# Performance work log

Hardware: AMD Instinct MI355X
Metric: run time of the kernel (lower is better)

The kernel has to match this reference:

```python
import jax, jax.numpy as jnp
import numpy as np

EPS = 1e-5  # torch nn.LayerNorm default eps
DIST_CUTOFF = 10.0


def _ln(x, g, b):
    m = jnp.mean(x, axis=-1, keepdims=True)
    v = jnp.mean((x - m) ** 2, axis=-1, keepdims=True)
    return (x - m) * jax.lax.rsqrt(v + EPS) * g + b


def setup_inputs() -> dict:
    key = jax.random.key(0)
    ks = iter(jax.random.split(key, 48))
    L, B, N, D, H = 4, 1, 256, 128, 512
    IN = D + N  # 384 == node_dim + edge_dim + node_dim under the consistency constraint
    r = lambda *s: jax.random.normal(next(ks), s, jnp.float32) * 0.02
    return dict(
        nodes=jax.random.normal(next(ks), (B, N, D), jnp.float32),
        coords=jax.random.normal(next(ks), (B, N, 3), jnp.float32),
        ee_w=r(1, D), ee_b=jnp.zeros(D), ee_g=jnp.ones(D), ee_bt=jnp.zeros(D),
        nu1_w=r(L, IN, H), nu1_b=jnp.zeros((L, H)), nu_g=jnp.ones((L, H)), nu_bt=jnp.zeros((L, H)),
        nu2_w=r(L, H, D), nu2_b=jnp.zeros((L, D)),
        eu1_w=r(L, IN, H), eu1_b=jnp.zeros((L, H)), eu_g=jnp.ones((L, H)), eu_bt=jnp.zeros((L, H)),
        eu2_w=r(L, H, D), eu2_b=jnp.zeros((L, D)),
        sp1_w=r(D, H), sp1_b=jnp.zeros(H), sp_g=jnp.ones(H), sp_bt=jnp.zeros(H),
        sp2_w=r(H, 3), sp2_b=jnp.zeros(3),
        no1_w=r(D, H), no1_b=jnp.zeros(H), no_g=jnp.ones(H), no_bt=jnp.zeros(H),
        no2_w=r(H, D), no2_b=jnp.zeros(D),
    )


def reference(nodes, coords, ee_w, ee_b, ee_g, ee_bt,
              nu1_w, nu1_b, nu_g, nu_bt, nu2_w, nu2_b,
              eu1_w, eu1_b, eu_g, eu_bt, eu2_w, eu2_b,
              sp1_w, sp1_b, sp_g, sp_bt, sp2_w, sp2_b,
              no1_w, no1_b, no_g, no_bt, no2_w, no2_b):
    B, N, D = nodes.shape
    # initialize_edges: pairwise distances -> edge embedding + adjacency
    diff = coords[:, :, None, :] - coords[:, None, :, :]           # [B,N,N,3]
    sq = jnp.sum(diff * diff, axis=-1)                              # [B,N,N]
    dist = jnp.where(sq > 0, jnp.sqrt(jnp.where(sq > 0, sq, 1.0)), 0.0)
    adj = (dist < DIST_CUTOFF).astype(nodes.dtype)                  # [B,N,N]
    edges = jax.nn.relu(_ln(dist[..., None] @ ee_w + ee_b, ee_g, ee_bt))  # [B,N,N,D]

    def step(carry, p):
        nd, ed = carry
        w1n, b1n, gn, btn, w2n, b2n, w1e, b1e, ge, bte, w2e, b2e = p
        # messages: einsum('bijk,bik->bij', edges*adj[...,None], nodes)
        msgs = adj * jnp.einsum('bijk,bik->bij', ed, nd)            # [B,N,N]
        ni = jnp.concatenate([nd, msgs], axis=-1)                    # [B,N,D+N]
        nd_new = nd + jax.nn.relu(_ln(ni @ w1n + b1n, gn, btn)) @ w2n + b2n
        pairs = jnp.concatenate([
            jnp.broadcast_to(nd[:, :, None, :], (B, N, N, D)),
            jnp.broadcast_to(nd[:, None, :, :], (B, N, N, D))], axis=-1)  # [B,N,N,2D]
        ei = jnp.concatenate([ed, pairs], axis=-1)                   # [B,N,N,3D]
        ed_new = ed + jax.nn.relu(_ln(ei @ w1e + b1e, ge, bte)) @ w2e + b2e
        return (nd_new, ed_new), None

    (nd, _ed), _ = jax.lax.scan(
        step, (nodes, edges),
        (nu1_w, nu1_b, nu_g, nu_bt, nu2_w, nu2_b,
         eu1_w, eu1_b, eu_g, eu_bt, eu2_w, eu2_b))

    nodes_out = jax.nn.relu(_ln(nd @ no1_w + no1_b, no_g, no_bt)) @ no2_w + no2_b
    coords_pred = jax.nn.relu(_ln(nodes_out @ sp1_w + sp1_b, sp_g, sp_bt)) @ sp2_w + sp2_b
    return nodes_out, coords_pred
```

## Files before the change

kernel.cpp:

```cpp
#include <hip/hip_runtime.h>

#define LNEPS 1e-5f

typedef unsigned short ushort_t;
typedef __attribute__((ext_vector_type(8))) short short8;
typedef __attribute__((ext_vector_type(4))) float f32x4;

__device__ inline unsigned short f2b(float f) {
    union { float f; unsigned int u; } c; c.f = f;
    unsigned int u = c.u;
    unsigned int r = (u + 0x7FFFu + ((u >> 16) & 1u)) >> 16;
    return (unsigned short)r;
}

__global__ void k_convw(const float* __restrict__ w1, const float* __restrict__ w2,
                        ushort_t* __restrict__ w1P, ushort_t* __restrict__ w2P) {
    int idx = blockIdx.x * 256 + threadIdx.x;
    if (idx < 65536) {
        int l = idx >> 14, r = idx & 16383;
        int c = r >> 9;  r &= 511;
        int kb = r >> 6, lane = r & 63;
        int col = c * 16 + (lane & 15);
        int k0 = kb * 32 + (lane >> 4) * 8;
        ushort_t o[8];
        #pragma unroll
        for (int e = 0; e < 8; ++e) {
            int kl = k0 + e;
            int row = kl < 128 ? kl : kl + 128;
            o[e] = f2b(w1[((size_t)l * 384 + row) * 512 + col]);
        }
        *(uint4*)(w1P + (size_t)idx * 8) = *(uint4*)o;
    }
    if (idx < 32768) {
        int l = idx >> 13, r = idx & 8191;
        int c2 = r >> 10; r &= 1023;
        int kbg = r >> 6, lane = r & 63;
        int col = c2 * 16 + (lane & 15);
        int k0 = kbg * 32 + (lane >> 4) * 8;
        ushort_t o[8];
        #pragma unroll
        for (int e = 0; e < 8; ++e)
            o[e] = f2b(w2[((size_t)l * 512 + k0 + e) * 128 + col]);
        *(uint4*)(w2P + (size_t)idx * 8) = *(uint4*)o;
    }
}

__global__ void k_init(const float* __restrict__ coords,
                       const float* __restrict__ ee_w, const float* __restrict__ ee_b,
                       const float* __restrict__ ee_g, const float* __restrict__ ee_bt,
                       float* __restrict__ ed, float* __restrict__ adjf) {
    int r = blockIdx.x * 4 + (threadIdx.x >> 6);
    int lane = threadIdx.x & 63;
    int i = r >> 8, j = r & 255;
    float dx = coords[i * 3 + 0] - coords[j * 3 + 0];
    float dy = coords[i * 3 + 1] - coords[j * 3 + 1];
    float dz = coords[i * 3 + 2] - coords[j * 3 + 2];
    float sq = dx * dx + dy * dy + dz * dz;
    float dist = sq > 0.f ? sqrtf(sq) : 0.f;
    if (lane == 0) adjf[r] = dist < 10.f ? 1.f : 0.f;
    float e0 = dist * ee_w[lane] + ee_b[lane];
    float e1 = dist * ee_w[lane + 64] + ee_b[lane + 64];
    float s = e0 + e1, q = e0 * e0 + e1 * e1;
    #pragma unroll
    for (int off = 1; off < 64; off <<= 1) {
        s += __shfl_xor(s, off, 64);
        q += __shfl_xor(q, off, 64);
    }
    float mean = s * (1.f / 128.f);
    float var = q * (1.f / 128.f) - mean * mean;
    float rs = rsqrtf(var + LNEPS);
    ed[(size_t)r * 128 + lane]      = fmaxf((e0 - mean) * rs * ee_g[lane] + ee_bt[lane], 0.f);
    ed[(size_t)r * 128 + lane + 64] = fmaxf((e1 - mean) * rs * ee_g[lane + 64] + ee_bt[lane + 64], 0.f);
}

__global__ __launch_bounds__(512) void k_pre(
    const float* __restrict__ nd, const float* __restrict__ W1,
    const float* __restrict__ b1,
    float* __restrict__ cI, ushort_t* __restrict__ ndb) {
    __shared__ float ndl[128];
    int p = blockIdx.x, t = threadIdx.x;
    if (t < 128) {
        float v = nd[(size_t)p * 128 + t];
        ndl[t] = v;
        ndb[(size_t)p * 128 + t] = f2b(v);
    }
    __syncthreads();
    const float* wm = W1 + (size_t)128 * 512 + t;
    float a1 = b1[t];
    #pragma unroll 4
    for (int k = 0; k < 128; ++k) a1 += ndl[k] * wm[(size_t)k * 512];
    cI[(size_t)p * 512 + t] = a1;
}

__global__ void k_msgs(const float* __restrict__ ed, const float* __restrict__ nd,
                       const float* __restrict__ adjf, float* __restrict__ msgs) {
    int r = blockIdx.x * 4 + (threadIdx.x >> 6);
    int lane = threadIdx.x & 63;
    int i = r >> 8;
    const float* er = ed + (size_t)r * 128;
    const float* nr = nd + (size_t)i * 128;
    float sum = er[lane] * nr[lane] + er[lane + 64] * nr[lane + 64];
    #pragma unroll
    for (int off = 1; off < 64; off <<= 1) sum += __shfl_xor(sum, off, 64);
    if (lane == 0) msgs[r] = adjf[r] * sum;
}

__global__ __launch_bounds__(512) void k_mlp(
    const float* __restrict__ in0, int w0, const float* __restrict__ in1, int w1n,
    const float* __restrict__ W1, const float* __restrict__ b1,
    const float* __restrict__ g, const float* __restrict__ bt,
    const float* __restrict__ W2, const float* __restrict__ b2, int O,
    const float* __restrict__ res, float* __restrict__ out) {
    __shared__ float ni[384];
    __shared__ float hsh[512];
    __shared__ float part[4][128];
    __shared__ float red[16];
    int row = blockIdx.x;
    int t = threadIdx.x;
    int K = w0 + w1n;
    if (t < w0) ni[t] = in0[(size_t)row * w0 + t];
    else if (t < K) ni[t] = in1[(size_t)row * w1n + (t - w0)];
    __syncthreads();
    float acc = b1[t];
    #pragma unroll 4
    for (int k = 0; k < K; ++k) acc += ni[k] * W1[(size_t)k * 512 + t];
    float s = acc, q = acc * acc;
    #pragma unroll
    for (int off = 1; off < 64; off <<= 1) {
        s += __shfl_xor(s, off, 64);
        q += __shfl_xor(q, off, 64);
    }
    int wv = t >> 6;
    if ((t & 63) == 0) { red[wv] = s; red[8 + wv] = q; }
    __syncthreads();
    float S = 0.f, Q = 0.f;
    #pragma unroll
    for (int w = 0; w < 8; ++w) { S += red[w]; Q += red[8 + w]; }
    float mean = S * (1.f / 512.f);
    float var = Q * (1.f / 512.f) - mean * mean;
    float rs = rsqrtf(var + LNEPS);
    hsh[t] = fmaxf((acc - mean) * rs * g[t] + bt[t], 0.f);
    __syncthreads();
    int qd = t >> 7, c = t & 127;
    float pacc = 0.f;
    if (c < O) {
        #pragma unroll 4
        for (int kk = 0; kk < 128; ++kk)
            pacc += hsh[qd * 128 + kk] * W2[(size_t)(qd * 128 + kk) * O + c];
    }
    part[qd][c] = pacc;
    __syncthreads();
    if (t < O) {
        float v = part[0][t] + part[1][t] + part[2][t] + part[3][t] + b2[t];
        if (res) v += res[(size_t)row * O + t];
        out[(size_t)row * O + t] = v;
    }
}

__global__ __launch_bounds__(512, 4) void k_edge(
    float* ed, const ushort_t* __restrict__ ndb, const float* __restrict__ cIg,
    const ushort_t* __restrict__ w1P,
    const float* __restrict__ g, const float* __restrict__ bt,
    const ushort_t* __restrict__ w2P, const float* __restrict__ b2) {
    __shared__ char smem[70144];
    const int tid = threadIdx.x;
    const int w = tid >> 6, lane = tid & 63;
    const int l15 = lane & 15, lhi = lane >> 4;
    const int rbase = blockIdx.x * 64;
    const int ib = rbase >> 8;
    const int jbase = rbase & 255;

    #pragma unroll
    for (int it = 0; it < 4; ++it) {
        int c = tid + it * 512;
        int row = c >> 5, q = c & 31;
        uint4 pk;
        if (q < 16) {
            const float4* sp = (const float4*)(ed + (size_t)(rbase + row) * 128 + q * 8);
            float4 v0 = sp[0], v1 = sp[1];
            pk.x = (unsigned)f2b(v0.x) | ((unsigned)f2b(v0.y) << 16);
            pk.y = (unsigned)f2b(v0.z) | ((unsigned)f2b(v0.w) << 16);
            pk.z = (unsigned)f2b(v1.x) | ((unsigned)f2b(v1.y) << 16);
            pk.w = (unsigned)f2b(v1.z) | ((unsigned)f2b(v1.w) << 16);
        } else {
            pk = *(const uint4*)(ndb + (size_t)(jbase + row) * 128 + (q - 16) * 8);
        }
        *(uint4*)(smem + row * 512 + ((q ^ (row & 7)) * 16)) = pk;
    }
    __syncthreads();

    f32x4 acc[4][4];
    f32x4 zero = {0.f, 0.f, 0.f, 0.f};
    #pragma unroll
    for (int m = 0; m < 4; ++m)
        #pragma unroll
        for (int n = 0; n < 4; ++n) acc[m][n] = zero;

    const int cw = w * 64;
    #pragma unroll 2
    for (int kb = 0; kb < 8; ++kb) {
        short8 a[4];
        #pragma unroll
        for (int m = 0; m < 4; ++m) {
            int row = m * 16 + l15;
            a[m] = *(const short8*)(smem + row * 512 + (((kb * 4 + lhi) ^ (row & 7)) * 16));
        }
        #pragma unroll
        for (int n = 0; n < 4; ++n) {
            short8 b = *(const short8*)(w1P + ((((w * 4 + n) * 8 + kb) << 6) + lane) * 8);
            #pragma unroll
            for (int m = 0; m < 4; ++m)
                acc[m][n] = __builtin_amdgcn_mfma_f32_16x16x32_bf16(a[m], b, acc[m][n], 0, 0, 0);
        }
    }

    float* red = (float*)(smem + 65536);
    float* stats = (float*)(smem + 69632);
    {
        float ci[4];
        #pragma unroll
        for (int n = 0; n < 4; ++n) ci[n] = cIg[(size_t)ib * 512 + cw + n * 16 + l15];
        #pragma unroll
        for (int m = 0; m < 4; ++m) {
            float s[4] = {0.f, 0.f, 0.f, 0.f}, q[4] = {0.f, 0.f, 0.f, 0.f};
            #pragma unroll
            for (int n = 0; n < 4; ++n)
                #pragma unroll
                for (int e = 0; e < 4; ++e) {
                    float v = acc[m][n][e] + ci[n];
                    acc[m][n][e] = v;
                    s[e] += v; q[e] += v * v;
                }
            #pragma unroll
            for (int off = 1; off < 16; off <<= 1)
                #pragma unroll
                for (int e = 0; e < 4; ++e) {
                    s[e] += __shfl_xor(s[e], off, 64);
                    q[e] += __shfl_xor(q[e], off, 64);
                }
            if (l15 == 0) {
                #pragma unroll
                for (int e = 0; e < 4; ++e) {
                    int row = m * 16 + lhi * 4 + e;
                    red[(w * 64 + row) * 2 + 0] = s[e];
                    red[(w * 64 + row) * 2 + 1] = q[e];
                }
            }
        }
    }
    __syncthreads();
    if (tid < 64) {
        float S = 0.f, Q = 0.f;
        #pragma unroll
        for (int ww = 0; ww < 8; ++ww) {
            S += red[(ww * 64 + tid) * 2 + 0];
            Q += red[(ww * 64 + tid) * 2 + 1];
        }
        float mean = S * (1.f / 512.f);
        float var = Q * (1.f / 512.f) - mean * mean;
        stats[tid * 2 + 0] = mean;
        stats[tid * 2 + 1] = rsqrtf(var + LNEPS);
    }
    __syncthreads();

    {
        float gg[4], bb[4];
        #pragma unroll
        for (int n = 0; n < 4; ++n) {
            gg[n] = g[cw + n * 16 + l15];
            bb[n] = bt[cw + n * 16 + l15];
        }
        #pragma unroll
        for (int m = 0; m < 4; ++m)
            #pragma unroll
            for (int e = 0; e < 4; ++e) {
                int row = m * 16 + lhi * 4 + e;
                float mean = stats[row * 2 + 0];
                float rs = stats[row * 2 + 1];
                #pragma unroll
                for (int n = 0; n < 4; ++n) {
                    float v = fmaxf((acc[m][n][e] - mean) * rs * gg[n] + bb[n], 0.f);
                    int p = cw + n * 16 + l15;
                    int addr = row * 1024 + (((p >> 3) ^ (row & 7)) * 16) + (p & 7) * 2;
                    *(ushort_t*)(smem + addr) = f2b(v);
                }
            }
    }
    __syncthreads();

    const int rt = w >> 1, ch2 = w & 1;
    f32x4 acc2[4];
    #pragma unroll
    for (int n2 = 0; n2 < 4; ++n2) acc2[n2] = zero;
    const int arow = rt * 16 + l15;
    #pragma unroll 2
    for (int kbg = 0; kbg < 16; ++kbg) {
        short8 a = *(const short8*)(smem + arow * 1024 + (((kbg * 4 + lhi) ^ (arow & 7)) * 16));
        #pragma unroll
        for (int n2 = 0; n2 < 4; ++n2) {
            int c2g = ch2 * 4 + n2;
            short8 b = *(const short8*)(w2P + (((c2g * 16 + kbg) << 6) + lane) * 8);
            acc2[n2] = __builtin_amdgcn_mfma_f32_16x16x32_bf16(a, b, acc2[n2], 0, 0, 0);
        }
    }

    #pragma unroll
    for (int n2 = 0; n2 < 4; ++n2) {
        int col = ch2 * 64 + n2 * 16 + l15;
        float bc = b2[col];
        #pragma unroll
        for (int e = 0; e < 4; ++e) {
            int row = rt * 16 + lhi * 4 + e;
            size_t off = (size_t)(rbase + row) * 128 + col;
            ed[off] = acc2[n2][e] + bc + ed[off];
        }
    }
}

extern "C" void kernel_launch(void* const* d_in, const int* in_sizes, int n_in,
                              void* d_out, int out_size, void* d_ws, size_t ws_size,
                              hipStream_t stream) {
    const float* nodes  = (const float*)d_in[0];
    const float* coords = (const float*)d_in[1];
    const float* ee_w   = (const float*)d_in[2];
    const float* ee_b   = (const float*)d_in[3];
    const float* ee_g   = (const float*)d_in[4];
    const float* ee_bt  = (const float*)d_in[5];
    const float* nu1_w  = (const float*)d_in[6];
    const float* nu1_b  = (const float*)d_in[7];
    const float* nu_g   = (const float*)d_in[8];
    const float* nu_bt  = (const float*)d_in[9];
    const float* nu2_w  = (const float*)d_in[10];
    const float* nu2_b  = (const float*)d_in[11];
    const float* eu1_w  = (const float*)d_in[12];
    const float* eu1_b  = (const float*)d_in[13];
    const float* eu_g   = (const float*)d_in[14];
    const float* eu_bt  = (const float*)d_in[15];
    const float* eu2_w  = (const float*)d_in[16];
    const float* eu2_b  = (const float*)d_in[17];
    const float* sp1_w  = (const float*)d_in[18];
    const float* sp1_b  = (const float*)d_in[19];
    const float* sp_g   = (const float*)d_in[20];
    const float* sp_bt  = (const float*)d_in[21];
    const float* sp2_w  = (const float*)d_in[22];
    const float* sp2_b  = (const float*)d_in[23];
    const float* no1_w  = (const float*)d_in[24];
    const float* no1_b  = (const float*)d_in[25];
    const float* no_g   = (const float*)d_in[26];
    const float* no_bt  = (const float*)d_in[27];
    const float* no2_w  = (const float*)d_in[28];
    const float* no2_b  = (const float*)d_in[29];

    char* p = (char*)d_ws;
    float* ed      = (float*)p;     p += (size_t)65536 * 128 * 4;
    float* ndA     = (float*)p;     p += 256 * 128 * 4;
    float* ndB     = (float*)p;     p += 256 * 128 * 4;
    ushort_t* ndb  = (ushort_t*)p;  p += 256 * 128 * 2;
    float* msgs    = (float*)p;     p += 65536 * 4;
    float* adjf    = (float*)p;     p += 65536 * 4;
    float* cI      = (float*)p;     p += 256 * 512 * 4;
    ushort_t* w1P  = (ushort_t*)p;  p += (size_t)4 * 131072 * 2;
    ushort_t* w2P  = (ushort_t*)p;  p += (size_t)4 * 65536 * 2;

    k_convw<<<256, 256, 0, stream>>>(eu1_w, eu2_w, w1P, w2P);
    k_init<<<16384, 256, 0, stream>>>(coords, ee_w, ee_b, ee_g, ee_bt, ed, adjf);

    const float* nd_cur = nodes;
    float* nd_bufs[2] = {ndA, ndB};
    for (int l = 0; l < 4; ++l) {
        float* nd_next = nd_bufs[l & 1];
        k_pre<<<256, 512, 0, stream>>>(nd_cur, eu1_w + (size_t)l * 384 * 512,
                                       eu1_b + l * 512, cI, ndb);
        k_msgs<<<16384, 256, 0, stream>>>(ed, nd_cur, adjf, msgs);
        k_mlp<<<256, 512, 0, stream>>>(nd_cur, 128, msgs, 256,
            nu1_w + (size_t)l * 384 * 512, nu1_b + l * 512, nu_g + l * 512, nu_bt + l * 512,
            nu2_w + (size_t)l * 512 * 128, nu2_b + l * 128, 128, nd_cur, nd_next);
        k_edge<<<1024, 512, 0, stream>>>(ed, ndb, cI,
            w1P + (size_t)l * 131072, eu_g + l * 512, eu_bt + l * 512,
            w2P + (size_t)l * 65536, eu2_b + l * 128);
        nd_cur = nd_next;
    }

    float* out_nodes  = (float*)d_out;
    float* out_coords = out_nodes + 32768;
    k_mlp<<<256, 512, 0, stream>>>(nd_cur, 128, nullptr, 0,
        no1_w, no1_b, no_g, no_bt, no2_w, no2_b, 128, nullptr, out_nodes);
    k_mlp<<<256, 512, 0, stream>>>(out_nodes, 128, nullptr, 0,
        sp1_w, sp1_b, sp_g, sp_bt, sp2_w, sp2_b, 3, nullptr, out_coords);
}
```

Before: 625.6 us.

## Fuse message computation into edge kernel and keep bf16 edge copy

Removes the separate per-layer message kernel. The next layer's messages are now computed in the edge-update epilogue from the freshly written edges and the new node features, and the first layer's messages in the init kernel. A bf16 shadow copy of the edge tensor is kept, so the edge kernel loads bf16 directly instead of converting fp32. The MFMA operands are swapped so each lane holds four contiguous columns, which allows float4 epilogue loads and stores. The cost is extra bf16 writes per layer plus an extra buffer, in exchange for dropping a full fp32 edge read pass per layer.

Result: slower. 639.7 us (+2.3%).

```diff
diff --git a/kernel.cpp b/kernel.cpp
--- a/kernel.cpp
+++ b/kernel.cpp
@@ -45,10 +45,11 @@
     }
 }
 
-__global__ void k_init(const float* __restrict__ coords,
+__global__ void k_init(const float* __restrict__ coords, const float* __restrict__ nodes,
                        const float* __restrict__ ee_w, const float* __restrict__ ee_b,
                        const float* __restrict__ ee_g, const float* __restrict__ ee_bt,
-                       float* __restrict__ ed, float* __restrict__ adjf) {
+                       float* __restrict__ ed, ushort_t* __restrict__ edb,
+                       float* __restrict__ adjf, float* __restrict__ msgs) {
     int r = blockIdx.x * 4 + (threadIdx.x >> 6);
     int lane = threadIdx.x & 63;
     int i = r >> 8, j = r & 255;
@@ -57,7 +58,8 @@
     float dz = coords[i * 3 + 2] - coords[j * 3 + 2];
     float sq = dx * dx + dy * dy + dz * dz;
     float dist = sq > 0.f ? sqrtf(sq) : 0.f;
-    if (lane == 0) adjf[r] = dist < 10.f ? 1.f : 0.f;
+    float adjv = dist < 10.f ? 1.f : 0.f;
+    if (lane == 0) adjf[r] = adjv;
     float e0 = dist * ee_w[lane] + ee_b[lane];
     float e1 = dist * ee_w[lane + 64] + ee_b[lane + 64];
     float s = e0 + e1, q = e0 * e0 + e1 * e1;
@@ -69,8 +71,16 @@
     float mean = s * (1.f / 128.f);
     float var = q * (1.f / 128.f) - mean * mean;
     float rs = rsqrtf(var + LNEPS);
-    ed[(size_t)r * 128 + lane]      = fmaxf((e0 - mean) * rs * ee_g[lane] + ee_bt[lane], 0.f);
-    ed[(size_t)r * 128 + lane + 64] = fmaxf((e1 - mean) * rs * ee_g[lane + 64] + ee_bt[lane + 64], 0.f);
+    float e0r = fmaxf((e0 - mean) * rs * ee_g[lane] + ee_bt[lane], 0.f);
+    float e1r = fmaxf((e1 - mean) * rs * ee_g[lane + 64] + ee_bt[lane + 64], 0.f);
+    ed[(size_t)r * 128 + lane]       = e0r;
+    ed[(size_t)r * 128 + lane + 64]  = e1r;
+    edb[(size_t)r * 128 + lane]      = f2b(e0r);
+    edb[(size_t)r * 128 + lane + 64] = f2b(e1r);
+    float d = e0r * nodes[(i << 7) + lane] + e1r * nodes[(i << 7) + 64 + lane];
+    #pragma unroll
+    for (int off = 1; off < 64; off <<= 1) d += __shfl_xor(d, off, 64);
+    if (lane == 0) msgs[r] = adjv * d;
 }
 
 __global__ __launch_bounds__(512) void k_pre(
@@ -90,19 +100,6 @@
     #pragma unroll 4
     for (int k = 0; k < 128; ++k) a1 += ndl[k] * wm[(size_t)k * 512];
     cI[(size_t)p * 512 + t] = a1;
-}
-
-__global__ void k_msgs(const float* __restrict__ ed, const float* __restrict__ nd,
-                       const float* __restrict__ adjf, float* __restrict__ msgs) {
-    int r = blockIdx.x * 4 + (threadIdx.x >> 6);
-    int lane = threadIdx.x & 63;
-    int i = r >> 8;
-    const float* er = ed + (size_t)r * 128;
-    const float* nr = nd + (size_t)i * 128;
-    float sum = er[lane] * nr[lane] + er[lane + 64] * nr[lane + 64];
-    #pragma unroll
-    for (int off = 1; off < 64; off <<= 1) sum += __shfl_xor(sum, off, 64);
-    if (lane == 0) msgs[r] = adjf[r] * sum;
 }
 
 __global__ __launch_bounds__(512) void k_mlp(
@@ -158,10 +155,12 @@
 }
 
 __global__ __launch_bounds__(512, 4) void k_edge(
-    float* ed, const ushort_t* __restrict__ ndb, const float* __restrict__ cIg,
-    const ushort_t* __restrict__ w1P,
+    float* ed, ushort_t* edb, const ushort_t* __restrict__ ndb,
+    const float* __restrict__ cIg, const ushort_t* __restrict__ w1P,
     const float* __restrict__ g, const float* __restrict__ bt,
-    const ushort_t* __restrict__ w2P, const float* __restrict__ b2) {
+    const ushort_t* __restrict__ w2P, const float* __restrict__ b2,
+    const float* __restrict__ ndn, const float* __restrict__ adjf,
+    float* __restrict__ msgs) {
     __shared__ char smem[70144];
     const int tid = threadIdx.x;
     const int w = tid >> 6, lane = tid & 63;
@@ -175,16 +174,8 @@
         int c = tid + it * 512;
         int row = c >> 5, q = c & 31;
         uint4 pk;
-        if (q < 16) {
-            const float4* sp = (const float4*)(ed + (size_t)(rbase + row) * 128 + q * 8);
-            float4 v0 = sp[0], v1 = sp[1];
-            pk.x = (unsigned)f2b(v0.x) | ((unsigned)f2b(v0.y) << 16);
-            pk.y = (unsigned)f2b(v0.z) | ((unsigned)f2b(v0.w) << 16);
-            pk.z = (unsigned)f2b(v1.x) | ((unsigned)f2b(v1.y) << 16);
-            pk.w = (unsigned)f2b(v1.z) | ((unsigned)f2b(v1.w) << 16);
-        } else {
-            pk = *(const uint4*)(ndb + (size_t)(jbase + row) * 128 + (q - 16) * 8);
-        }
+        if (q < 16) pk = *(const uint4*)(edb + (size_t)(rbase + row) * 128 + q * 8);
+        else        pk = *(const uint4*)(ndb + (size_t)(jbase + row) * 128 + (q - 16) * 8);
         *(uint4*)(smem + row * 512 + ((q ^ (row & 7)) * 16)) = pk;
     }
     __syncthreads();
@@ -210,41 +201,38 @@
             short8 b = *(const short8*)(w1P + ((((w * 4 + n) * 8 + kb) << 6) + lane) * 8);
             #pragma unroll
             for (int m = 0; m < 4; ++m)
-                acc[m][n] = __builtin_amdgcn_mfma_f32_16x16x32_bf16(a[m], b, acc[m][n], 0, 0, 0);
+                acc[m][n] = __builtin_amdgcn_mfma_f32_16x16x32_bf16(b, a[m], acc[m][n], 0, 0, 0);
         }
     }
 
     float* red = (float*)(smem + 65536);
     float* stats = (float*)(smem + 69632);
     {
-        float ci[4];
-        #pragma unroll
-        for (int n = 0; n < 4; ++n) ci[n] = cIg[(size_t)ib * 512 + cw + n * 16 + l15];
+        float4 ci[4];
+        #pragma unroll
+        for (int n = 0; n < 4; ++n)
+            ci[n] = *(const float4*)(cIg + (size_t)ib * 512 + cw + n * 16 + lhi * 4);
         #pragma unroll
         for (int m = 0; m < 4; ++m) {
-            float s[4] = {0.f, 0.f, 0.f, 0.f}, q[4] = {0.f, 0.f, 0.f, 0.f};
+            float s = 0.f, q = 0.f;
             #pragma unroll
-            for (int n = 0; n < 4; ++n)
-                #pragma unroll
-                for (int e = 0; e < 4; ++e) {
-                    float v = acc[m][n][e] + ci[n];
-                    acc[m][n][e] = v;
-                    s[e] += v; q[e] += v * v;
-                }
-            #pragma unroll
-            for (int off = 1; off < 16; off <<= 1)
-                #pragma unroll
-                for (int e = 0; e < 4; ++e) {
-                    s[e] += __shfl_xor(s[e], off, 64);
-                    q[e] += __shfl_xor(q[e], off, 64);
-                }
-            if (l15 == 0) {
-                #pragma unroll
-                for (int e = 0; e < 4; ++e) {
-                    int row = m * 16 + lhi * 4 + e;
-                    red[(w * 64 + row) * 2 + 0] = s[e];
-                    red[(w * 64 + row) * 2 + 1] = q[e];
-                }
+            for (int n = 0; n < 4; ++n) {
+                float v0 = acc[m][n][0] + ci[n].x;
+                float v1 = acc[m][n][1] + ci[n].y;
+                float v2 = acc[m][n][2] + ci[n].z;
+                float v3 = acc[m][n][3] + ci[n].w;
+                acc[m][n][0] = v0; acc[m][n][1] = v1;
+                acc[m][n][2] = v2; acc[m][n][3] = v3;
+                s += v0 + v1 + v2 + v3;
+                q += v0 * v0 + v1 * v1 + v2 * v2 + v3 * v3;
+            }
+            s += __shfl_xor(s, 16, 64);
+            s += __shfl_xor(s, 32, 64);
+            q += __shfl_xor(q, 16, 64);
+            q += __shfl_xor(q, 32, 64);
+            if (lhi == 0) {
+                red[(w * 64 + m * 16 + l15) * 2 + 0] = s;
+                red[(w * 64 + m * 16 + l15) * 2 + 1] = q;
             }
         }
     }
@@ -264,27 +252,31 @@
     __syncthreads();
 
     {
-        float gg[4], bb[4];
+        float4 gg[4], bb[4];
         #pragma unroll
         for (int n = 0; n < 4; ++n) {
-            gg[n] = g[cw + n * 16 + l15];
-            bb[n] = bt[cw + n * 16 + l15];
-        }
-        #pragma unroll
-        for (int m = 0; m < 4; ++m)
+            gg[n] = *(const float4*)(g + cw + n * 16 + lhi * 4);
+            bb[n] = *(const float4*)(bt + cw + n * 16 + lhi * 4);
+        }
+        #pragma unroll
+        for (int m = 0; m < 4; ++m) {
+            int row = m * 16 + l15;
+            float mean = stats[row * 2 + 0];
+            float rs = stats[row * 2 + 1];
             #pragma unroll
-            for (int e = 0; e < 4; ++e) {
-                int row = m * 16 + lhi * 4 + e;
-                float mean = stats[row * 2 + 0];
-                float rs = stats[row * 2 + 1];
-                #pragma unroll
-                for (int n = 0; n < 4; ++n) {
-                    float v = fmaxf((acc[m][n][e] - mean) * rs * gg[n] + bb[n], 0.f);
-                    int p = cw + n * 16 + l15;
-                    int addr = row * 1024 + (((p >> 3) ^ (row & 7)) * 16) + (p & 7) * 2;
-                    *(ushort_t*)(smem + addr) = f2b(v);
-                }
+            for (int n = 0; n < 4; ++n) {
+                float v0 = fmaxf((acc[m][n][0] - mean) * rs * gg[n].x + bb[n].x, 0.f);
+                float v1 = fmaxf((acc[m][n][1] - mean) * rs * gg[n].y + bb[n].y, 0.f);
+                float v2 = fmaxf((acc[m][n][2] - mean) * rs * gg[n].z + bb[n].z, 0.f);
+                float v3 = fmaxf((acc[m][n][3] - mean) * rs * gg[n].w + bb[n].w, 0.f);
+                int p0 = cw + n * 16 + lhi * 4;
+                int addr = row * 1024 + ((((p0 >> 3) ^ (row & 7))) * 16) + (p0 & 7) * 2;
+                uint2 pk;
+                pk.x = (unsigned)f2b(v0) | ((unsigned)f2b(v1) << 16);
+                pk.y = (unsigned)f2b(v2) | ((unsigned)f2b(v3) << 16);
+                *(uint2*)(smem + addr) = pk;
             }
+        }
     }
     __syncthreads();
 
@@ -298,23 +290,40 @@
         short8 a = *(const short8*)(smem + arow * 1024 + (((kbg * 4 + lhi) ^ (arow & 7)) * 16));
         #pragma unroll
         for (int n2 = 0; n2 < 4; ++n2) {
-            int c2g = ch2 * 4 + n2;
-            short8 b = *(const short8*)(w2P + (((c2g * 16 + kbg) << 6) + lane) * 8);
-            acc2[n2] = __builtin_amdgcn_mfma_f32_16x16x32_bf16(a, b, acc2[n2], 0, 0, 0);
-        }
-    }
-
-    #pragma unroll
-    for (int n2 = 0; n2 < 4; ++n2) {
-        int col = ch2 * 64 + n2 * 16 + l15;
-        float bc = b2[col];
-        #pragma unroll
-        for (int e = 0; e < 4; ++e) {
-            int row = rt * 16 + lhi * 4 + e;
-            size_t off = (size_t)(rbase + row) * 128 + col;
-            ed[off] = acc2[n2][e] + bc + ed[off];
-        }
-    }
+            short8 b = *(const short8*)(w2P + ((((ch2 * 4 + n2) * 16 + kbg) << 6) + lane) * 8);
+            acc2[n2] = __builtin_amdgcn_mfma_f32_16x16x32_bf16(b, a, acc2[n2], 0, 0, 0);
+        }
+    }
+
+    float partial = 0.f;
+    {
+        const int row = rt * 16 + l15;
+        #pragma unroll
+        for (int n2 = 0; n2 < 4; ++n2) {
+            int col0 = ch2 * 64 + n2 * 16 + lhi * 4;
+            size_t goff = (size_t)(rbase + row) * 128 + col0;
+            float4 r4 = *(const float4*)(ed + goff);
+            float4 b4 = *(const float4*)(b2 + col0);
+            float4 n4 = *(const float4*)(ndn + (size_t)ib * 128 + col0);
+            float o0 = acc2[n2][0] + b4.x + r4.x;
+            float o1 = acc2[n2][1] + b4.y + r4.y;
+            float o2 = acc2[n2][2] + b4.z + r4.z;
+            float o3 = acc2[n2][3] + b4.w + r4.w;
+            float4 o4 = {o0, o1, o2, o3};
+            *(float4*)(ed + goff) = o4;
+            uint2 pk;
+            pk.x = (unsigned)f2b(o0) | ((unsigned)f2b(o1) << 16);
+            pk.y = (unsigned)f2b(o2) | ((unsigned)f2b(o3) << 16);
+            *(uint2*)(edb + goff) = pk;
+            partial += o0 * n4.x + o1 * n4.y + o2 * n4.z + o3 * n4.w;
+        }
+    }
+    partial += __shfl_xor(partial, 16, 64);
+    partial += __shfl_xor(partial, 32, 64);
+    float* msum = (float*)(smem + 65536);
+    if (lhi == 0) msum[ch2 * 64 + rt * 16 + l15] = partial;
+    __syncthreads();
+    if (tid < 64) msgs[rbase + tid] = adjf[rbase + tid] * (msum[tid] + msum[64 + tid]);
 }
 
 extern "C" void kernel_launch(void* const* d_in, const int* in_sizes, int n_in,
@@ -353,6 +362,7 @@
 
     char* p = (char*)d_ws;
     float* ed      = (float*)p;     p += (size_t)65536 * 128 * 4;
+    ushort_t* edb  = (ushort_t*)p;  p += (size_t)65536 * 128 * 2;
     float* ndA     = (float*)p;     p += 256 * 128 * 4;
     float* ndB     = (float*)p;     p += 256 * 128 * 4;
     ushort_t* ndb  = (ushort_t*)p;  p += 256 * 128 * 2;
@@ -363,7 +373,8 @@
     ushort_t* w2P  = (ushort_t*)p;  p += (size_t)4 * 65536 * 2;
 
     k_convw<<<256, 256, 0, stream>>>(eu1_w, eu2_w, w1P, w2P);
-    k_init<<<16384, 256, 0, stream>>>(coords, ee_w, ee_b, ee_g, ee_bt, ed, adjf);
+    k_init<<<16384, 256, 0, stream>>>(coords, nodes, ee_w, ee_b, ee_g, ee_bt,
+                                      ed, edb, adjf, msgs);
 
     const float* nd_cur = nodes;
     float* nd_bufs[2] = {ndA, ndB};
@@ -371,13 +382,13 @@
         float* nd_next = nd_bufs[l & 1];
         k_pre<<<256, 512, 0, stream>>>(nd_cur, eu1_w + (size_t)l * 384 * 512,
                                        eu1_b + l * 512, cI, ndb);
-        k_msgs<<<16384, 256, 0, stream>>>(ed, nd_cur, adjf, msgs);
         k_mlp<<<256, 512, 0, stream>>>(nd_cur, 128, msgs, 256,
             nu1_w + (size_t)l * 384 * 512, nu1_b + l * 512, nu_g + l * 512, nu_bt + l * 512,
             nu2_w + (size_t)l * 512 * 128, nu2_b + l * 128, 128, nd_cur, nd_next);
-        k_edge<<<1024, 512, 0, stream>>>(ed, ndb, cI,
+        k_edge<<<1024, 512, 0, stream>>>(ed, edb, ndb, cI,
             w1P + (size_t)l * 131072, eu_g + l * 512, eu_bt + l * 512,
-            w2P + (size_t)l * 65536, eu2_b + l * 128);
+            w2P + (size_t)l * 65536, eu2_b + l * 128,
+            nd_next, adjf, msgs);
         nd_cur = nd_next;
     }
 
```
